# Kernel optimization log

Hardware: AMD Instinct MI355X
Metric: run time of the kernel (lower is better)

## Reference

```python
import jax, jax.numpy as jnp
import numpy as np

V, E, H, K, B, T = 50000, 128, 256, 9, 128, 512
HD = H // 2  # hidden per direction


def setup_inputs() -> dict:
    key = jax.random.key(0)
    ks = jax.random.split(key, 16)
    s = 0.1
    inp = {
        "x": jax.random.randint(ks[0], (B, T), 0, V),
        "emb": jax.random.normal(ks[1], (V, E), jnp.float32) * 0.02,
        "w_ih_f": jax.random.normal(ks[2], (4 * HD, E), jnp.float32) * s,
        "w_hh_f": jax.random.normal(ks[3], (4 * HD, HD), jnp.float32) * s,
        "b_ih_f": jax.random.normal(ks[4], (4 * HD,), jnp.float32) * s,
        "b_hh_f": jax.random.normal(ks[5], (4 * HD,), jnp.float32) * s,
        "w_ih_b": jax.random.normal(ks[6], (4 * HD, E), jnp.float32) * s,
        "w_hh_b": jax.random.normal(ks[7], (4 * HD, HD), jnp.float32) * s,
        "b_ih_b": jax.random.normal(ks[8], (4 * HD,), jnp.float32) * s,
        "b_hh_b": jax.random.normal(ks[9], (4 * HD,), jnp.float32) * s,
        "W_tag": jax.random.normal(ks[10], (K, H), jnp.float32) * s,
        "b_tag": jax.random.normal(ks[11], (K,), jnp.float32) * s,
        "start_trans": jax.random.normal(ks[12], (K,), jnp.float32) * s,
        "end_trans": jax.random.normal(ks[13], (K,), jnp.float32) * s,
        "trans": jax.random.normal(ks[14], (K, K), jnp.float32) * s,
    }
    return inp


def _lstm_dir(xs, w_ih, w_hh, b_ih, b_hh, reverse):
    # xs: [T, B, E]; PyTorch gate order: i, f, g, o
    Bsz = xs.shape[1]
    hd = w_hh.shape[1]
    b = b_ih + b_hh

    def step(carry, x_t):
        h, c = carry
        gates = x_t @ w_ih.T + h @ w_hh.T + b  # [B, 4*hd]
        i, f, g, o = jnp.split(gates, 4, axis=-1)
        i = jax.nn.sigmoid(i)
        f = jax.nn.sigmoid(f)
        g = jnp.tanh(g)
        o = jax.nn.sigmoid(o)
        c = f * c + i * g
        h = o * jnp.tanh(c)
        return (h, c), h

    init = (jnp.zeros((Bsz, hd), xs.dtype), jnp.zeros((Bsz, hd), xs.dtype))
    _, hs = jax.lax.scan(step, init, xs, reverse=reverse)
    return hs  # [T, B, hd], time-ordered


def _viterbi(emissions, start_trans, end_trans, trans):
    # emissions: [T, B, K]; returns best tag path [B, T] (torchcrf decode, no mask)
    score0 = start_trans[None, :] + emissions[0]  # [B, K]

    def step(score, emis_t):
        # score[b, i] + trans[i, j] -> best over i
        cand = score[:, :, None] + trans[None, :, :]  # [B, K, K]
        bp = jnp.argmax(cand, axis=1)                 # [B, K] best prev tag
        best = jnp.max(cand, axis=1)
        return best + emis_t, bp

    final_score, bps = jax.lax.scan(step, score0, emissions[1:])  # bps: [T-1, B, K]
    final_score = final_score + end_trans[None, :]
    last_tag = jnp.argmax(final_score, axis=-1)  # [B]

    def back(tag, bp):
        prev = jnp.take_along_axis(bp, tag[:, None], axis=1)[:, 0]
        return prev, prev

    _, path = jax.lax.scan(back, last_tag, bps, reverse=True)  # [T-1, B]
    tags = jnp.concatenate([path, last_tag[None, :]], axis=0)  # [T, B]
    return tags.T.astype(jnp.int32)  # [B, T]


def reference(x, emb, w_ih_f, w_hh_f, b_ih_f, b_hh_f,
              w_ih_b, w_hh_b, b_ih_b, b_hh_b,
              W_tag, b_tag, start_trans, end_trans, trans):
    xt = x.T                        # [T, B]
    e = emb[xt]                     # [T, B, E] embedding gather
    h_f = _lstm_dir(e, w_ih_f, w_hh_f, b_ih_f, b_hh_f, reverse=False)
    h_b = _lstm_dir(e, w_ih_b, w_hh_b, b_ih_b, b_hh_b, reverse=True)
    h = jnp.concatenate([h_f, h_b], axis=-1)  # [T, B, H]
    # dropout is identity at inference
    emissions = h @ W_tag.T + b_tag           # [T, B, K]
    return _viterbi(emissions, start_trans, end_trans, trans)
```

## Files before the change

### kernel.cpp

```cpp
#include <hip/hip_runtime.h>
#include <math.h>

#define TT 512
#define BB 128
#define KK 9

__device__ __forceinline__ float fast_sigmoid(float x) {
    const float LOG2E = 1.4426950408889634f;
    float e = __builtin_amdgcn_exp2f(-x * LOG2E);
    return __builtin_amdgcn_rcpf(1.0f + e);
}
__device__ __forceinline__ float fast_tanh(float x) {
    const float LOG2E = 1.4426950408889634f;
    float a = fabsf(x);
    float e = __builtin_amdgcn_exp2f(-2.0f * a * LOG2E);
    float t = (1.0f - e) * __builtin_amdgcn_rcpf(1.0f + e);
    return copysignf(t, x);
}

__global__ __launch_bounds__(512, 2) void lstm_fused(
    const int* __restrict__ x, const float* __restrict__ emb,
    const float* __restrict__ w_ih_f, const float* __restrict__ w_ih_b,
    const float* __restrict__ b_ih_f, const float* __restrict__ b_hh_f,
    const float* __restrict__ b_ih_b, const float* __restrict__ b_hh_b,
    float* __restrict__ buf2,
    const float* __restrict__ w_hh_f, const float* __restrict__ w_hh_b,
    float* __restrict__ h_all,
    float* __restrict__ h_state, float* __restrict__ c_state,
    const float* __restrict__ W_tag, const float* __restrict__ b_tag,
    const float* __restrict__ start_trans, const float* __restrict__ end_trans,
    const float* __restrict__ trans,
    float* __restrict__ emB, unsigned* __restrict__ flags,
    int* __restrict__ out,
    int t0f, int t0b, int C, int init, int tail)
{
    const int dir = blockIdx.x >> 7;
    const int b   = blockIdx.x & 127;
    const int j   = threadIdx.x;

    __shared__ __align__(16) float h_lds[2][128];
    __shared__ __align__(16) float wt_s[KK * 132];
    __shared__ __align__(16) float em_s[TT * KK];
    __shared__ __align__(16) float h_tile[64 * 132];
    __shared__ unsigned char bp[TT][KK];
    __shared__ int bj_s;

    unsigned snap = 0u;
    if (tail && dir == 0 && j == 0)
        snap = __hip_atomic_load(&flags[b], __ATOMIC_RELAXED, __HIP_MEMORY_SCOPE_AGENT);

    const int t0 = dir ? t0b : t0f;

    {
        int*   x_s = (int*)wt_s;
        float* As2 = em_s;
        float* Bs2 = h_tile;
        const float* wih = dir ? w_ih_b : w_ih_f;
        const float* bi  = dir ? b_ih_b : b_ih_f;
        const float* bh  = dir ? b_hh_b : b_hh_f;
        float* myb = buf2 + (size_t)(dir * BB + b) * C * 512;

        for (int f = j; f < C; f += 512) x_s[f] = x[b * TT + t0 + f];
        __syncthreads();

        const int ty  = j >> 5;
        const int tx  = j & 31;
        const int Atr = j >> 2;
        const int Aq  = (j & 3) * 8;
        const int Bgr = j >> 1;
        const int Bq  = (j & 1) * 16;

        const int ntg = C >> 7;
        for (int gg = 0; gg < 2; gg++) {
            const int g0 = gg * 256 + tx * 4;
            const int g1 = g0 + 128;
            float bias0[4], bias1[4];
            #pragma unroll
            for (int u = 0; u < 4; u++) {
                bias0[u] = bi[g0 + u] + bh[g0 + u];
                bias1[u] = bi[g1 + u] + bh[g1 + u];
            }
            const float* bBase = wih + (size_t)(gg * 256 + Bgr) * 128;

            for (int tg = 0; tg < ntg; tg++) {
                float acc[8][8];
                #pragma unroll
                for (int i = 0; i < 8; i++)
                    #pragma unroll
                    for (int jj = 0; jj < 8; jj++) acc[i][jj] = 0.0f;

                const int tokA = x_s[tg * 128 + Atr];
                const float* aBase = emb + (size_t)tokA * 128;

                float4 aP0 = *(const float4*)(aBase + Aq);
                float4 aP1 = *(const float4*)(aBase + Aq + 4);
                float4 bP0 = *(const float4*)(bBase + Bq);
                float4 bP1 = *(const float4*)(bBase + Bq + 4);
                float4 bP2 = *(const float4*)(bBase + Bq + 8);
                float4 bP3 = *(const float4*)(bBase + Bq + 12);

                for (int kc = 0; kc < 128; kc += 32) {
                    __syncthreads();
                    As2[(Aq + 0) * 132 + Atr] = aP0.x;
                    As2[(Aq + 1) * 132 + Atr] = aP0.y;
                    As2[(Aq + 2) * 132 + Atr] = aP0.z;
                    As2[(Aq + 3) * 132 + Atr] = aP0.w;
                    As2[(Aq + 4) * 132 + Atr] = aP1.x;
                    As2[(Aq + 5) * 132 + Atr] = aP1.y;
                    As2[(Aq + 6) * 132 + Atr] = aP1.z;
                    As2[(Aq + 7) * 132 + Atr] = aP1.w;
                    Bs2[(Bq + 0) * 260 + Bgr] = bP0.x;
                    Bs2[(Bq + 1) * 260 + Bgr] = bP0.y;
                    Bs2[(Bq + 2) * 260 + Bgr] = bP0.z;
                    Bs2[(Bq + 3) * 260 + Bgr] = bP0.w;
                    Bs2[(Bq + 4) * 260 + Bgr] = bP1.x;
                    Bs2[(Bq + 5) * 260 + Bgr] = bP1.y;
                    Bs2[(Bq + 6) * 260 + Bgr] = bP1.z;
                    Bs2[(Bq + 7) * 260 + Bgr] = bP1.w;
                    Bs2[(Bq + 8) * 260 + Bgr] = bP2.x;
                    Bs2[(Bq + 9) * 260 + Bgr] = bP2.y;
                    Bs2[(Bq + 10) * 260 + Bgr] = bP2.z;
                    Bs2[(Bq + 11) * 260 + Bgr] = bP2.w;
                    Bs2[(Bq + 12) * 260 + Bgr] = bP3.x;
                    Bs2[(Bq + 13) * 260 + Bgr] = bP3.y;
                    Bs2[(Bq + 14) * 260 + Bgr] = bP3.z;
                    Bs2[(Bq + 15) * 260 + Bgr] = bP3.w;
                    __syncthreads();
                    if (kc + 32 < 128) {
                        aP0 = *(const float4*)(aBase + kc + 32 + Aq);
                        aP1 = *(const float4*)(aBase + kc + 32 + Aq + 4);
                        bP0 = *(const float4*)(bBase + kc + 32 + Bq);
                        bP1 = *(const float4*)(bBase + kc + 32 + Bq + 4);
                        bP2 = *(const float4*)(bBase + kc + 32 + Bq + 8);
                        bP3 = *(const float4*)(bBase + kc + 32 + Bq + 12);
                    }
                    #pragma unroll 8
                    for (int k = 0; k < 32; k++) {
                        float4 af0 = *(const float4*)&As2[k * 132 + ty * 8];
                        float4 af1 = *(const float4*)&As2[k * 132 + ty * 8 + 4];
                        float4 bf0 = *(const float4*)&Bs2[k * 260 + tx * 4];
                        float4 bf1 = *(const float4*)&Bs2[k * 260 + 128 + tx * 4];
                        float a_[8] = {af0.x, af0.y, af0.z, af0.w,
                                       af1.x, af1.y, af1.z, af1.w};
                        float b_[8] = {bf0.x, bf0.y, bf0.z, bf0.w,
                                       bf1.x, bf1.y, bf1.z, bf1.w};
                        #pragma unroll
                        for (int i = 0; i < 8; i++)
                            #pragma unroll
                            for (int jj = 0; jj < 8; jj++)
                                acc[i][jj] += a_[i] * b_[jj];
                    }
                }
                #pragma unroll
                for (int i = 0; i < 8; i++) {
                    const int tl = tg * 128 + ty * 8 + i;
                    float* o = myb + (size_t)tl * 512;
                    float4 v0, v1;
                    v0.x = acc[i][0] + bias0[0]; v0.y = acc[i][1] + bias0[1];
                    v0.z = acc[i][2] + bias0[2]; v0.w = acc[i][3] + bias0[3];
                    v1.x = acc[i][4] + bias1[0]; v1.y = acc[i][5] + bias1[1];
                    v1.z = acc[i][6] + bias1[2]; v1.w = acc[i][7] + bias1[3];
                    *(float4*)(o + g0) = v0;
                    *(float4*)(o + g1) = v1;
                }
            }
        }
    }

    const int w_  = j >> 6;
    const int l   = j & 63;
    const int m   = l >> 2;
    const int q   = l & 3;
    const int k   = w_ * 16 + m;
    const int r   = q * 128 + k;

    const float* whh = dir ? w_hh_b : w_hh_f;
    float wR[128];
    #pragma unroll
    for (int qq = 0; qq < 32; qq++) {
        float4 v = *(const float4*)(whh + (size_t)r * 128 + qq * 4);
        wR[4*qq+0] = v.x; wR[4*qq+1] = v.y; wR[4*qq+2] = v.z; wR[4*qq+3] = v.w;
    }

    float c;
    if (init) {
        c = 0.0f;
        if (q == 0) h_lds[0][k] = 0.0f;
    } else {
        c = c_state[((size_t)dir * 128 + b) * 128 + k];
        if (q == 0) h_lds[0][k] = h_state[((size_t)dir * 128 + b) * 128 + k];
    }
    __syncthreads();

    const int  tl0   = dir ? (C - 1) : 0;
    const long lstep = dir ? -(long)512 : (long)512;

    const float* xp = buf2 + ((size_t)(dir * BB + b) * C + tl0) * 512 + r;
    float xw = *xp;
    float h_reg = 0.0f;

    float* hdst = h_all + (size_t)(dir * BB + b) * TT * 128;

    for (int s = 0; s < C; s++) {
        const int t = t0 + (dir ? (C - 1 - s) : s);
        const int p = s & 1;
        const float* hprev = h_lds[p];

        float a0 = 0.f, a1 = 0.f, a2 = 0.f, a3 = 0.f;
        #pragma unroll
        for (int qq = 0; qq < 32; qq++) {
            float4 h4 = *(const float4*)&hprev[4 * qq];
            a0 += wR[4*qq+0] * h4.x;
            a1 += wR[4*qq+1] * h4.y;
            a2 += wR[4*qq+2] * h4.z;
            a3 += wR[4*qq+3] * h4.w;
        }
        float pre = xw + ((a0 + a1) + (a2 + a3));

        float act = (q == 2) ? fast_tanh(pre) : fast_sigmoid(pre);

        float f_ = __shfl_xor(act, 1);
        float g_ = __shfl_xor(act, 2);
        float o_ = __shfl_xor(act, 3);

        c = f_ * c + act * g_;
        h_reg = o_ * fast_tanh(c);
        if (q == 0) h_lds[p ^ 1][k] = h_reg;

        __syncthreads();

        if (s + 1 < C) { xp += lstep; xw = *xp; }
        if (q == 0)
            hdst[(size_t)t * 128 + k] = h_reg;
    }

    if (q == 0) {
        h_state[((size_t)dir * 128 + b) * 128 + k] = h_reg;
        c_state[((size_t)dir * 128 + b) * 128 + k] = c;
    }

    if (!tail) return;

    for (int f = j; f < KK * 128; f += 512)
        wt_s[(f >> 7) * 132 + (f & 127)] = W_tag[(f >> 7) * 256 + dir * 128 + (f & 127)];

    float* emdst = emB + (size_t)b * TT * KK;

    for (int tile = 0; tile < TT / 64; tile++) {
        const int tb = tile * 64;
        __syncthreads();
        #pragma unroll
        for (int it = 0; it < 4; it++) {
            const int f4 = it * 512 + j;
            const int tr = f4 >> 5;
            const int c4 = (f4 & 31) * 4;
            float4 v = *(const float4*)(hdst + (size_t)(tb + tr) * 128 + c4);
            *(float4*)&h_tile[tr * 132 + c4] = v;
        }
        __syncthreads();
        for (int task = j; task < 64 * KK; task += 512) {
            const int tl = task / 9;
            const int kk = task - tl * 9;
            const float* hp = &h_tile[tl * 132];
            const float* wp = &wt_s[kk * 132];
            float acc = 0.0f;
            #pragma unroll
            for (int i4 = 0; i4 < 32; i4++) {
                float4 h4 = *(const float4*)(hp + i4 * 4);
                float4 w4 = *(const float4*)(wp + i4 * 4);
                acc += h4.x * w4.x + h4.y * w4.y + h4.z * w4.z + h4.w * w4.w;
            }
            if (dir == 1) emdst[(size_t)tb * KK + task] = acc;
            else          em_s[tb * KK + task] = acc;
        }
    }
    __syncthreads();

    if (dir == 1) {
        if (j == 0) {
            __threadfence();
            __hip_atomic_fetch_add(&flags[b], 1u, __ATOMIC_RELEASE,
                                   __HIP_MEMORY_SCOPE_AGENT);
        }
        return;
    }

    if (j == 0) {
        while (__hip_atomic_load(&flags[b], __ATOMIC_ACQUIRE,
                                 __HIP_MEMORY_SCOPE_AGENT) == snap)
            __builtin_amdgcn_s_sleep(1);
    }
    __syncthreads();
    for (int f = j; f < TT * KK; f += 512)
        em_s[f] += emdst[f] + b_tag[f % KK];
    __syncthreads();

    if (j < 64) {
        const int lane = j;

        float trans_col[KK];
        float score = -1e30f;
        if (lane < KK) {
            #pragma unroll
            for (int i = 0; i < KK; i++) trans_col[i] = trans[i * KK + lane];
            score = start_trans[lane] + em_s[lane];
        }

        float em_cur = (lane < KK) ? em_s[KK + lane] : 0.0f;
        for (int t = 1; t < TT; t++) {
            float em_next = (t + 1 < TT && lane < KK) ? em_s[(t + 1) * KK + lane] : 0.0f;

            float my = (lane < KK) ? score : -1e30f;
            float cand[KK];
            #pragma unroll
            for (int i = 0; i < KK; i++) cand[i] = __shfl(my, i) + trans_col[i];

            float v01, v23, v45, v67, v03, v47, v07, vb_;
            int   i01, i23, i45, i67, i03, i47, i07, ib_;
            {
                bool gt;
                gt = cand[1] > cand[0]; v01 = gt ? cand[1] : cand[0]; i01 = gt ? 1 : 0;
                gt = cand[3] > cand[2]; v23 = gt ? cand[3] : cand[2]; i23 = gt ? 3 : 2;
                gt = cand[5] > cand[4]; v45 = gt ? cand[5] : cand[4]; i45 = gt ? 5 : 4;
                gt = cand[7] > cand[6]; v67 = gt ? cand[7] : cand[6]; i67 = gt ? 7 : 6;
                gt = v23 > v01; v03 = gt ? v23 : v01; i03 = gt ? i23 : i01;
                gt = v67 > v45; v47 = gt ? v67 : v45; i47 = gt ? i67 : i45;
                gt = v47 > v03; v07 = gt ? v47 : v03; i07 = gt ? i47 : i03;
                gt = cand[8] > v07; vb_ = gt ? cand[8] : v07; ib_ = gt ? 8 : i07;
            }

            if (lane < KK) {
                bp[t][lane] = (unsigned char)ib_;
                score = vb_ + em_cur;
            }
            em_cur = em_next;
        }

        float fin = (lane < KK) ? (score + end_trans[lane]) : -1e30f;
        float farr[KK];
        #pragma unroll
        for (int jx = 0; jx < KK; jx++) farr[jx] = __shfl(fin, jx);
        float v01, v23, v45, v67, v03, v47, v07, vb_;
        int   i01, i23, i45, i67, i03, i47, i07, bj;
        {
            bool gt;
            gt = farr[1] > farr[0]; v01 = gt ? farr[1] : farr[0]; i01 = gt ? 1 : 0;
            gt = farr[3] > farr[2]; v23 = gt ? farr[3] : farr[2]; i23 = gt ? 3 : 2;
            gt = farr[5] > farr[4]; v45 = gt ? farr[5] : farr[4]; i45 = gt ? 5 : 4;
            gt = farr[7] > farr[6]; v67 = gt ? farr[7] : farr[6]; i67 = gt ? 7 : 6;
            gt = v23 > v01; v03 = gt ? v23 : v01; i03 = gt ? i23 : i01;
            gt = v67 > v45; v47 = gt ? v67 : v45; i47 = gt ? i67 : i45;
            gt = v47 > v03; v07 = gt ? v47 : v03; i07 = gt ? i47 : i03;
            gt = farr[8] > v07; vb_ = gt ? farr[8] : v07; bj = gt ? 8 : i07;
        }

        if (lane == 0) {
            bj_s = bj;
            out[b * TT + (TT - 1)] = bj;
        }
    }
    __syncthreads();

    {
        unsigned char* mA = (unsigned char*)h_tile;
        unsigned char* mB = mA + TT * KK;
        #pragma unroll
        for (int i = 0; i < KK; i++)
            mA[j * KK + i] = (j >= 1) ? bp[j][i] : (unsigned char)0;
        __syncthreads();
        for (int kk = 1; kk < TT; kk <<= 1) {
            if (j >= 1) {
                if (j + kk < TT) {
                    #pragma unroll
                    for (int i = 0; i < KK; i++)
                        mB[j * KK + i] = mA[j * KK + mA[(j + kk) * KK + i]];
                } else {
                    #pragma unroll
                    for (int i = 0; i < KK; i++)
                        mB[j * KK + i] = mA[j * KK + i];
                }
            }
            __syncthreads();
            unsigned char* tmp = mA; mA = mB; mB = tmp;
        }
        if (j >= 1)
            out[b * TT + (j - 1)] = mA[j * KK + bj_s];
    }
}

extern "C" void kernel_launch(void* const* d_in, const int* in_sizes, int n_in,
                              void* d_out, int out_size, void* d_ws, size_t ws_size,
                              hipStream_t stream)
{
    const int*   x       = (const int*)  d_in[0];
    const float* emb     = (const float*)d_in[1];
    const float* w_ih_f  = (const float*)d_in[2];
    const float* w_hh_f  = (const float*)d_in[3];
    const float* b_ih_f  = (const float*)d_in[4];
    const float* b_hh_f  = (const float*)d_in[5];
    const float* w_ih_b  = (const float*)d_in[6];
    const float* w_hh_b  = (const float*)d_in[7];
    const float* b_ih_b  = (const float*)d_in[8];
    const float* b_hh_b  = (const float*)d_in[9];
    const float* W_tag   = (const float*)d_in[10];
    const float* b_tag   = (const float*)d_in[11];
    const float* start_t = (const float*)d_in[12];
    const float* end_t   = (const float*)d_in[13];
    const float* trans   = (const float*)d_in[14];
    int* out = (int*)d_out;

    const size_t em_elems    = (size_t)BB * TT * KK;
    const size_t state_elems = (size_t)2 * 128 * 128;
    const size_t hall_elems  = (size_t)2 * BB * TT * 128;

    int C = 128;
    const int cands[3] = {512, 256, 128};
    for (int ci = 0; ci < 3; ci++) {
        size_t need = ((size_t)2 * cands[ci] * BB * 512
                       + em_elems + 2 * state_elems + hall_elems) * sizeof(float)
                      + 1024;
        if (ws_size >= need) { C = cands[ci]; break; }
    }

    float* buf2    = (float*)d_ws;
    float* emB     = buf2 + (size_t)2 * C * BB * 512;
    float* h_state = emB + em_elems;
    float* c_state = h_state + state_elems;
    float* h_all   = c_state + state_elems;
    unsigned* flags = (unsigned*)(h_all + hall_elems);

    const int rounds = TT / C;
    for (int r = 0; r < rounds; r++) {
        const int t0f = r * C;
        const int t0b = TT - (r + 1) * C;
        lstm_fused<<<dim3(256), dim3(512), 0, stream>>>(
            x, emb, w_ih_f, w_ih_b, b_ih_f, b_hh_f, b_ih_b, b_hh_b,
            buf2, w_hh_f, w_hh_b, h_all,
            h_state, c_state,
            W_tag, b_tag, start_t, end_t, trans,
            emB, flags, out,
            t0f, t0b, C, (r == 0) ? 1 : 0, (r == rounds - 1) ? 1 : 0);
    }
}
```

Before: 850.4 us.

## Reuse input-projection buffer for hidden states and compute emissions per chunk

Drops the separate h_all workspace. Each step's hidden state now goes into a slot of the per-chunk gate buffer (offset 384 within each 512-wide row, which has already been consumed). Emission projections are computed at the end of every chunk round rather than only in the tail round, and written to separate forward and backward emission buffers. The Viterbi block then sums them from global memory. This shrinks the workspace and may let a larger chunk size C be chosen, but it adds global emission writes for both directions and relies on that buffer slot being dead when overwritten.

```diff
diff --git a/kernel.cpp b/kernel.cpp
--- a/kernel.cpp
+++ b/kernel.cpp
@@ -25,13 +25,12 @@
     const float* __restrict__ b_ih_b, const float* __restrict__ b_hh_b,
     float* __restrict__ buf2,
     const float* __restrict__ w_hh_f, const float* __restrict__ w_hh_b,
-    float* __restrict__ h_all,
     float* __restrict__ h_state, float* __restrict__ c_state,
     const float* __restrict__ W_tag, const float* __restrict__ b_tag,
     const float* __restrict__ start_trans, const float* __restrict__ end_trans,
     const float* __restrict__ trans,
-    float* __restrict__ emB, unsigned* __restrict__ flags,
-    int* __restrict__ out,
+    float* __restrict__ emF, float* __restrict__ emB,
+    unsigned* __restrict__ flags, int* __restrict__ out,
     int t0f, int t0b, int C, int init, int tail)
 {
     const int dir = blockIdx.x >> 7;
@@ -50,6 +49,7 @@
         snap = __hip_atomic_load(&flags[b], __ATOMIC_RELAXED, __HIP_MEMORY_SCOPE_AGENT);
 
     const int t0 = dir ? t0b : t0f;
+    float* myb = buf2 + (size_t)(dir * BB + b) * C * 512;
 
     {
         int*   x_s = (int*)wt_s;
@@ -58,7 +58,6 @@
         const float* wih = dir ? w_ih_b : w_ih_f;
         const float* bi  = dir ? b_ih_b : b_ih_f;
         const float* bh  = dir ? b_hh_b : b_hh_f;
-        float* myb = buf2 + (size_t)(dir * BB + b) * C * 512;
 
         for (int f = j; f < C; f += 512) x_s[f] = x[b * TT + t0 + f];
         __syncthreads();
@@ -195,14 +194,12 @@
     const int  tl0   = dir ? (C - 1) : 0;
     const long lstep = dir ? -(long)512 : (long)512;
 
-    const float* xp = buf2 + ((size_t)(dir * BB + b) * C + tl0) * 512 + r;
+    const float* xp = myb + (size_t)tl0 * 512 + r;
     float xw = *xp;
     float h_reg = 0.0f;
 
-    float* hdst = h_all + (size_t)(dir * BB + b) * TT * 128;
-
     for (int s = 0; s < C; s++) {
-        const int t = t0 + (dir ? (C - 1 - s) : s);
+        const int sl = dir ? (C - 1 - s) : s;
         const int p = s & 1;
         const float* hprev = h_lds[p];
 
@@ -231,7 +228,7 @@
 
         if (s + 1 < C) { xp += lstep; xw = *xp; }
         if (q == 0)
-            hdst[(size_t)t * 128 + k] = h_reg;
+            myb[(size_t)sl * 512 + 384 + k] = h_reg;
     }
 
     if (q == 0) {
@@ -239,14 +236,12 @@
         c_state[((size_t)dir * 128 + b) * 128 + k] = c;
     }
 
-    if (!tail) return;
-
     for (int f = j; f < KK * 128; f += 512)
         wt_s[(f >> 7) * 132 + (f & 127)] = W_tag[(f >> 7) * 256 + dir * 128 + (f & 127)];
 
-    float* emdst = emB + (size_t)b * TT * KK;
-
-    for (int tile = 0; tile < TT / 64; tile++) {
+    float* emdst = (dir ? emB : emF) + (size_t)b * TT * KK;
+
+    for (int tile = 0; tile < C / 64; tile++) {
         const int tb = tile * 64;
         __syncthreads();
         #pragma unroll
@@ -254,7 +249,7 @@
             const int f4 = it * 512 + j;
             const int tr = f4 >> 5;
             const int c4 = (f4 & 31) * 4;
-            float4 v = *(const float4*)(hdst + (size_t)(tb + tr) * 128 + c4);
+            float4 v = *(const float4*)(myb + (size_t)(tb + tr) * 512 + 384 + c4);
             *(float4*)&h_tile[tr * 132 + c4] = v;
         }
         __syncthreads();
@@ -270,11 +265,12 @@
                 float4 w4 = *(const float4*)(wp + i4 * 4);
                 acc += h4.x * w4.x + h4.y * w4.y + h4.z * w4.z + h4.w * w4.w;
             }
-            if (dir == 1) emdst[(size_t)tb * KK + task] = acc;
-            else          em_s[tb * KK + task] = acc;
+            emdst[(size_t)(t0 + tb) * KK + task] = acc;
         }
     }
     __syncthreads();
+
+    if (!tail) return;
 
     if (dir == 1) {
         if (j == 0) {
@@ -291,8 +287,12 @@
             __builtin_amdgcn_s_sleep(1);
     }
     __syncthreads();
-    for (int f = j; f < TT * KK; f += 512)
-        em_s[f] += emdst[f] + b_tag[f % KK];
+    {
+        const float* eF = emF + (size_t)b * TT * KK;
+        const float* eB = emB + (size_t)b * TT * KK;
+        for (int f = j; f < TT * KK; f += 512)
+            em_s[f] = eF[f] + eB[f] + b_tag[f % KK];
+    }
     __syncthreads();
 
     if (j < 64) {
@@ -411,23 +411,22 @@
 
     const size_t em_elems    = (size_t)BB * TT * KK;
     const size_t state_elems = (size_t)2 * 128 * 128;
-    const size_t hall_elems  = (size_t)2 * BB * TT * 128;
 
     int C = 128;
     const int cands[3] = {512, 256, 128};
     for (int ci = 0; ci < 3; ci++) {
         size_t need = ((size_t)2 * cands[ci] * BB * 512
-                       + em_elems + 2 * state_elems + hall_elems) * sizeof(float)
+                       + 2 * em_elems + 2 * state_elems) * sizeof(float)
                       + 1024;
         if (ws_size >= need) { C = cands[ci]; break; }
     }
 
     float* buf2    = (float*)d_ws;
-    float* emB     = buf2 + (size_t)2 * C * BB * 512;
+    float* emF     = buf2 + (size_t)2 * C * BB * 512;
+    float* emB     = emF + em_elems;
     float* h_state = emB + em_elems;
     float* c_state = h_state + state_elems;
-    float* h_all   = c_state + state_elems;
-    unsigned* flags = (unsigned*)(h_all + hall_elems);
+    unsigned* flags = (unsigned*)(c_state + state_elems);
 
     const int rounds = TT / C;
     for (int r = 0; r < rounds; r++) {
@@ -435,10 +434,10 @@
         const int t0b = TT - (r + 1) * C;
         lstm_fused<<<dim3(256), dim3(512), 0, stream>>>(
             x, emb, w_ih_f, w_ih_b, b_ih_f, b_hh_f, b_ih_b, b_hh_b,
-            buf2, w_hh_f, w_hh_b, h_all,
+            buf2, w_hh_f, w_hh_b,
             h_state, c_state,
             W_tag, b_tag, start_t, end_t, trans,
-            emB, flags, out,
+            emF, emB, flags, out,
             t0f, t0b, C, (r == 0) ? 1 : 0, (r == rounds - 1) ? 1 : 0);
     }
 }
```

Measured after the change: 868.8 us. +2.2%, slower.
